# Performance work log

Measured on AMD Instinct MI355X. Metric: run time of the kernel, lower is better.

## Reference

```python
import jax, jax.numpy as jnp
import numpy as np

NUM_ENTITIES = 100000
NUM_RELATIONS = 8
HIDDEN = 128
N_NODES = 100000
N_EDGES = 500000


def setup_inputs() -> dict:
    key = jax.random.key(0)
    ks = jax.random.split(key, 10)
    scale = 1.0 / np.sqrt(HIDDEN)
    inp = {
        "x_ids": jax.random.randint(ks[0], (N_NODES,), 0, NUM_ENTITIES),
        "edge_index": jax.random.randint(ks[1], (2, N_EDGES), 0, N_NODES),
        "edge_type": jax.random.randint(ks[2], (N_EDGES,), 0, NUM_RELATIONS),
        "emb": jax.random.normal(ks[3], (NUM_ENTITIES, HIDDEN), jnp.float32),
        "W1": jax.random.normal(ks[4], (NUM_RELATIONS, HIDDEN, HIDDEN), jnp.float32) * scale,
        "root1": jax.random.normal(ks[5], (HIDDEN, HIDDEN), jnp.float32) * scale,
        "b1": jnp.zeros((HIDDEN,), jnp.float32),
        "W2": jax.random.normal(ks[6], (NUM_RELATIONS, HIDDEN, HIDDEN), jnp.float32) * scale,
        "root2": jax.random.normal(ks[7], (HIDDEN, HIDDEN), jnp.float32) * scale,
        "b2": jnp.zeros((HIDDEN,), jnp.float32),
    }
    return inp


def rgcn_conv(x, edge_index, edge_type, W, root, bias):
    # x: [N, d]; W: [R, d, d]; PyG RGCNConv with aggr='mean' (per-relation mean)
    N, d = x.shape
    R = W.shape[0]
    src, dst = edge_index[0], edge_index[1]
    # transform every node under every relation: [N, R, d]
    h = jnp.einsum('nd,rdf->nrf', x, W)
    msg = h[src, edge_type]                       # [E, d] gather per edge
    seg = dst * R + edge_type                     # composite (node, relation) segment id
    sums = jax.ops.segment_sum(msg, seg, num_segments=N * R)
    cnt = jax.ops.segment_sum(jnp.ones((msg.shape[0], 1), x.dtype), seg, num_segments=N * R)
    agg = (sums / jnp.maximum(cnt, 1.0)).reshape(N, R, d).sum(axis=1)
    return agg + x @ root + bias


def reference(x_ids, edge_index, edge_type, emb, W1, root1, b1, W2, root2, b2):
    x = emb[x_ids]                                # embedding lookup [N, d]
    x = rgcn_conv(x, edge_index, edge_type, W1, root1, b1)
    x = jax.nn.relu(x)
    x = rgcn_conv(x, edge_index, edge_type, W2, root2, b2)
    return jax.nn.sigmoid(x)
```

## Files before the change

kernel.cpp:

```cpp
#include <hip/hip_runtime.h>
#include <hip/hip_bf16.h>

#define HD 128
#define RNUM 8
#define SCAN_BS 2048

typedef __attribute__((ext_vector_type(8))) short short8;
typedef __attribute__((ext_vector_type(4))) float float4e;

__device__ __forceinline__ unsigned short f2bf(float f) {
    unsigned int u = __float_as_uint(f);
    u += 0x7fffu + ((u >> 16) & 1u);
    return (unsigned short)(u >> 16);
}

__device__ __forceinline__ void gload_lds16(const void* g, void* l) {
    __builtin_amdgcn_global_load_lds(
        (const __attribute__((address_space(1))) void*)g,
        (__attribute__((address_space(3))) void*)l, 16, 0, 0);
}

__global__ void zero_i(int* __restrict__ p, int n) {
    int g = blockIdx.x * blockDim.x + threadIdx.x;
    if (g < n) p[g] = 0;
}

__global__ void count_kernel(const int* __restrict__ ei, const int* __restrict__ et,
                             int* __restrict__ cnt, int E, int N) {
    int e = blockIdx.x * blockDim.x + threadIdx.x;
    if (e < E) atomicAdd(&cnt[et[e] * N + ei[E + e]], 1);
}

__global__ void scan1(const int* __restrict__ in, int* __restrict__ out,
                      int* __restrict__ bsum, int n) {
    __shared__ int s[256];
    const int tid = threadIdx.x;
    const int base = blockIdx.x * SCAN_BS + tid * 8;
    int v[8];
    int sum = 0;
#pragma unroll
    for (int j = 0; j < 8; j++) {
        int x = (base + j < n) ? in[base + j] : 0;
        v[j] = sum;
        sum += x;
    }
    s[tid] = sum;
    __syncthreads();
    for (int off = 1; off < 256; off <<= 1) {
        int tv = (tid >= off) ? s[tid - off] : 0;
        __syncthreads();
        if (tid >= off) s[tid] += tv;
        __syncthreads();
    }
    int excl = (tid > 0) ? s[tid - 1] : 0;
    if (tid == 255) bsum[blockIdx.x] = s[255];
#pragma unroll
    for (int j = 0; j < 8; j++)
        if (base + j < n) out[base + j] = v[j] + excl;
}

__global__ void scan2(int* __restrict__ bsum, int nb) {
    __shared__ int s[512];
    const int tid = threadIdx.x;
    s[tid] = (tid < nb) ? bsum[tid] : 0;
    __syncthreads();
    for (int off = 1; off < 512; off <<= 1) {
        int tv = (tid >= off) ? s[tid - off] : 0;
        __syncthreads();
        if (tid >= off) s[tid] += tv;
        __syncthreads();
    }
    if (tid < nb) bsum[tid] = (tid > 0) ? s[tid - 1] : 0;
}

__global__ void scan3(int* __restrict__ out, int* __restrict__ cur,
                      const int* __restrict__ bsum, int n) {
    const int base = blockIdx.x * SCAN_BS + threadIdx.x * 8;
    const int add = bsum[blockIdx.x];
#pragma unroll
    for (int j = 0; j < 8; j++) {
        int i = base + j;
        if (i < n) {
            int v = out[i] + add;
            out[i] = v;
            cur[i] = v;
        }
    }
}

__global__ void fill_kernel(const int* __restrict__ ei, const int* __restrict__ et,
                            const int* __restrict__ ids,
                            int* __restrict__ cur, int* __restrict__ col,
                            int* __restrict__ colE, int E, int N) {
    int e = blockIdx.x * blockDim.x + threadIdx.x;
    if (e < E) {
        int src = ei[e];
        int pos = atomicAdd(&cur[et[e] * N + ei[E + e]], 1);
        col[pos] = src;
        colE[pos] = ids[src];
    }
}

__global__ void wt_kernel(const float* __restrict__ W, unsigned short* __restrict__ WT,
                          int nmat) {
    int g = blockIdx.x * blockDim.x + threadIdx.x;
    if (g >= nmat * 16384) return;
    int mat = g >> 14;
    int d = (g >> 7) & 127;
    int f = g & 127;
    WT[mat * 16384 + f * 128 + d] = f2bf(W[g]);
}

template <bool HAS_IDX, int ACT>
__launch_bounds__(512, 4)
__global__ void rgcn_fused(const int* __restrict__ row_start, const int* __restrict__ col,
                           const int* __restrict__ ids, const float* __restrict__ x,
                           const unsigned short* __restrict__ WT,
                           const float* __restrict__ bias,
                           float* __restrict__ Cout, int N, int E) {
    __shared__ unsigned short As[128 * 128];
    __shared__ unsigned short Ws[128 * 128];

    const int tid = threadIdx.x;
    const int block0 = blockIdx.x * 128;
    const int w = tid >> 6;
    const int lane = tid & 63;
    const int ln15 = lane & 15;
    const int quad = lane >> 4;
    const int rowbase = (w & 1) * 64;
    const int colbase = (w >> 1) * 32;
    const int grp = tid >> 3;
    const int sub8 = tid & 7;

    float4e acc[4][2];
#pragma unroll
    for (int i = 0; i < 4; i++)
#pragma unroll
        for (int j = 0; j < 2; j++)
#pragma unroll
            for (int q = 0; q < 4; q++) acc[i][j][q] = 0.0f;

    for (int s = 0; s < 9; s++) {
        {
            const unsigned short* Wsrc = WT + s * 16384;
#pragma unroll
            for (int i = 0; i < 4; i++) {
                int c = i * 512 + tid;
                int f = c >> 4;
                int cc = c & 15;
                const void* src = (const void*)(Wsrc + f * 128 + ((cc ^ (f & 15)) << 3));
                int cbase = i * 512 + (tid & ~63);
                gload_lds16(src, (char*)Ws + (size_t)cbase * 16);
            }
        }
        if (s < RNUM) {
#pragma unroll 1
            for (int half = 0; half < 2; half++) {
                const int row = grp + half * 64;
                const int dst = block0 + row;
                float4e a0 = {0.f, 0.f, 0.f, 0.f};
                float4e a1 = {0.f, 0.f, 0.f, 0.f};
                float4e a2 = {0.f, 0.f, 0.f, 0.f};
                float4e a3 = {0.f, 0.f, 0.f, 0.f};
                float inv = 0.f;
                if (dst < N) {
                    int seg = s * N + dst;
                    int s0 = row_start[seg];
                    int s1 = (seg == RNUM * N - 1) ? E : row_start[seg + 1];
                    if (s1 > s0) inv = 1.0f / (float)(s1 - s0);
                    for (int e = s0; e < s1; e++) {
                        int c = col[e];
                        const float4e* xp = (const float4e*)(x + (size_t)c * HD + sub8 * 16);
                        a0 += xp[0];
                        a1 += xp[1];
                        a2 += xp[2];
                        a3 += xp[3];
                    }
                }
                a0 *= inv; a1 *= inv; a2 *= inv; a3 *= inv;
                uint4 o0, o1;
                o0.x = (unsigned int)f2bf(a0[0]) | ((unsigned int)f2bf(a0[1]) << 16);
                o0.y = (unsigned int)f2bf(a0[2]) | ((unsigned int)f2bf(a0[3]) << 16);
                o0.z = (unsigned int)f2bf(a1[0]) | ((unsigned int)f2bf(a1[1]) << 16);
                o0.w = (unsigned int)f2bf(a1[2]) | ((unsigned int)f2bf(a1[3]) << 16);
                o1.x = (unsigned int)f2bf(a2[0]) | ((unsigned int)f2bf(a2[1]) << 16);
                o1.y = (unsigned int)f2bf(a2[2]) | ((unsigned int)f2bf(a2[3]) << 16);
                o1.z = (unsigned int)f2bf(a3[0]) | ((unsigned int)f2bf(a3[1]) << 16);
                o1.w = (unsigned int)f2bf(a3[2]) | ((unsigned int)f2bf(a3[3]) << 16);
                const int ck0 = sub8 * 2;
                *(uint4*)&As[row * 128 + ((ck0 ^ (row & 15)) << 3)] = o0;
                *(uint4*)&As[row * 128 + (((ck0 + 1) ^ (row & 15)) << 3)] = o1;
            }
        } else {
#pragma unroll 1
            for (int half = 0; half < 2; half++) {
                const int row = grp + half * 64;
                const int dst = block0 + row;
                uint4 o0 = {0u, 0u, 0u, 0u}, o1 = {0u, 0u, 0u, 0u};
                if (dst < N) {
                    int srcn = HAS_IDX ? ids[dst] : dst;
                    const float* xp = x + (size_t)srcn * HD + sub8 * 16;
                    float4 v0 = *(const float4*)(xp);
                    float4 v1 = *(const float4*)(xp + 4);
                    float4 v2 = *(const float4*)(xp + 8);
                    float4 v3 = *(const float4*)(xp + 12);
                    o0.x = (unsigned int)f2bf(v0.x) | ((unsigned int)f2bf(v0.y) << 16);
                    o0.y = (unsigned int)f2bf(v0.z) | ((unsigned int)f2bf(v0.w) << 16);
                    o0.z = (unsigned int)f2bf(v1.x) | ((unsigned int)f2bf(v1.y) << 16);
                    o0.w = (unsigned int)f2bf(v1.z) | ((unsigned int)f2bf(v1.w) << 16);
                    o1.x = (unsigned int)f2bf(v2.x) | ((unsigned int)f2bf(v2.y) << 16);
                    o1.y = (unsigned int)f2bf(v2.z) | ((unsigned int)f2bf(v2.w) << 16);
                    o1.z = (unsigned int)f2bf(v3.x) | ((unsigned int)f2bf(v3.y) << 16);
                    o1.w = (unsigned int)f2bf(v3.z) | ((unsigned int)f2bf(v3.w) << 16);
                }
                const int ck0 = sub8 * 2;
                *(uint4*)&As[row * 128 + ((ck0 ^ (row & 15)) << 3)] = o0;
                *(uint4*)&As[row * 128 + (((ck0 + 1) ^ (row & 15)) << 3)] = o1;
            }
        }
        __syncthreads();

#pragma unroll
        for (int k0 = 0; k0 < 4; k0++) {
            short8 af[4], bf[2];
#pragma unroll
            for (int rt = 0; rt < 4; rt++) {
                int m = rowbase + rt * 16 + ln15;
                int ck = k0 * 4 + quad;
                af[rt] = *(const short8*)&As[m * 128 + ((ck ^ (m & 15)) << 3)];
            }
#pragma unroll
            for (int ct = 0; ct < 2; ct++) {
                int n = colbase + ct * 16 + ln15;
                int ck = k0 * 4 + quad;
                bf[ct] = *(const short8*)&Ws[n * 128 + ((ck ^ (n & 15)) << 3)];
            }
#pragma unroll
            for (int rt = 0; rt < 4; rt++)
#pragma unroll
                for (int ct = 0; ct < 2; ct++)
                    acc[rt][ct] = __builtin_amdgcn_mfma_f32_16x16x32_bf16(
                        af[rt], bf[ct], acc[rt][ct], 0, 0, 0);
        }
        __syncthreads();
    }

#pragma unroll
    for (int ct = 0; ct < 2; ct++) {
        int ncol = colbase + ct * 16 + ln15;
        float bv = bias[ncol];
#pragma unroll
        for (int rt = 0; rt < 4; rt++) {
#pragma unroll
            for (int rg = 0; rg < 4; rg++) {
                int rowg = block0 + rowbase + rt * 16 + quad * 4 + rg;
                if (rowg < N) {
                    float v = acc[rt][ct][rg] + bv;
                    v = (ACT == 0) ? fmaxf(v, 0.0f) : (1.0f / (1.0f + expf(-v)));
                    Cout[(size_t)rowg * HD + ncol] = v;
                }
            }
        }
    }
}

extern "C" void kernel_launch(void* const* d_in, const int* in_sizes, int n_in,
                              void* d_out, int out_size, void* d_ws, size_t ws_size,
                              hipStream_t stream) {
    const int*   x_ids = (const int*)d_in[0];
    const int*   ei    = (const int*)d_in[1];
    const int*   et    = (const int*)d_in[2];
    const float* emb   = (const float*)d_in[3];
    const float* W1    = (const float*)d_in[4];
    const float* root1 = (const float*)d_in[5];
    const float* b1    = (const float*)d_in[6];
    const float* W2    = (const float*)d_in[7];
    const float* root2 = (const float*)d_in[8];
    const float* b2    = (const float*)d_in[9];

    const int N = in_sizes[0];
    const int E = in_sizes[1] / 2;
    const int NS = RNUM * N;
    float* out = (float*)d_out;

    char* ws = (char*)d_ws;
    size_t off = 0;
    int* row_start = (int*)(ws + off); off += (size_t)NS * 4;
    int* col       = (int*)(ws + off); off += (size_t)E * 4;
    int* colE      = (int*)(ws + off); off += (size_t)E * 4;
    int* bsum      = (int*)(ws + off); off += 4096;
    unsigned short* WT = (unsigned short*)(ws + off); off += (size_t)18 * 16384 * 2;
    float* z       = (float*)(ws + off); off += (size_t)N * HD * 4;
    int* cur       = (int*)z;

    const int scanBlocks = (NS + SCAN_BS - 1) / SCAN_BS;
    const int layerGrid = (N + 127) / 128;

    zero_i<<<(NS + 255) / 256, 256, 0, stream>>>(cur, NS);
    count_kernel<<<(E + 255) / 256, 256, 0, stream>>>(ei, et, cur, E, N);
    scan1<<<scanBlocks, 256, 0, stream>>>(cur, row_start, bsum, NS);
    scan2<<<1, 512, 0, stream>>>(bsum, scanBlocks);
    scan3<<<scanBlocks, 256, 0, stream>>>(row_start, cur, bsum, NS);
    fill_kernel<<<(E + 255) / 256, 256, 0, stream>>>(ei, et, x_ids, cur, col, colE, E, N);

    wt_kernel<<<(8 * 16384 + 255) / 256, 256, 0, stream>>>(W1, WT, 8);
    wt_kernel<<<(1 * 16384 + 255) / 256, 256, 0, stream>>>(root1, WT + 8 * 16384, 1);
    wt_kernel<<<(8 * 16384 + 255) / 256, 256, 0, stream>>>(W2, WT + 9 * 16384, 8);
    wt_kernel<<<(1 * 16384 + 255) / 256, 256, 0, stream>>>(root2, WT + 17 * 16384, 1);

    rgcn_fused<true, 0><<<layerGrid, 512, 0, stream>>>(
        row_start, colE, x_ids, emb, WT, b1, z, N, E);
    rgcn_fused<false, 1><<<layerGrid, 512, 0, stream>>>(
        row_start, col, nullptr, z, WT + 9 * 16384, b2, out, N, E);
}
```

Before: 439.1 us.

## Gather bf16 features, shrink tiles to 64 rows, read weights directly from global

Converts the embedding table to bf16 in a pre-pass and writes the layer-1 output as bf16, so the per-edge neighbour gathers move half the bytes. The fused kernel now uses 64-row tiles with 256 threads and drops the LDS weight staging, reading B fragments straight from global/L2. The four weight-transpose launches are merged into one. The bf16 intermediate adds rounding error, and the extra conversion pass over the full embedding table (100k×128) costs bandwidth.

```diff
diff --git a/kernel.cpp b/kernel.cpp
--- a/kernel.cpp
+++ b/kernel.cpp
@@ -1,5 +1,4 @@
 #include <hip/hip_runtime.h>
-#include <hip/hip_bf16.h>
 
 #define HD 128
 #define RNUM 8
@@ -14,15 +13,28 @@
     return (unsigned short)(u >> 16);
 }
 
-__device__ __forceinline__ void gload_lds16(const void* g, void* l) {
-    __builtin_amdgcn_global_load_lds(
-        (const __attribute__((address_space(1))) void*)g,
-        (__attribute__((address_space(3))) void*)l, 16, 0, 0);
+__device__ __forceinline__ void acc2(float4e& a, unsigned int u, int i) {
+    a[i]     += __uint_as_float(u << 16);
+    a[i + 1] += __uint_as_float(u & 0xffff0000u);
 }
 
 __global__ void zero_i(int* __restrict__ p, int n) {
     int g = blockIdx.x * blockDim.x + threadIdx.x;
     if (g < n) p[g] = 0;
+}
+
+__global__ void tobf16_kernel(const float* __restrict__ in, unsigned short* __restrict__ out,
+                              long long n8) {
+    long long g = (long long)blockIdx.x * blockDim.x + threadIdx.x;
+    if (g >= n8) return;
+    const float4* p = (const float4*)(in + g * 8);
+    float4 v0 = p[0], v1 = p[1];
+    uint4 o;
+    o.x = (unsigned int)f2bf(v0.x) | ((unsigned int)f2bf(v0.y) << 16);
+    o.y = (unsigned int)f2bf(v0.z) | ((unsigned int)f2bf(v0.w) << 16);
+    o.z = (unsigned int)f2bf(v1.x) | ((unsigned int)f2bf(v1.y) << 16);
+    o.w = (unsigned int)f2bf(v1.z) | ((unsigned int)f2bf(v1.w) << 16);
+    *(uint4*)(out + g * 8) = o;
 }
 
 __global__ void count_kernel(const int* __restrict__ ei, const int* __restrict__ et,
@@ -101,62 +113,58 @@
     }
 }
 
-__global__ void wt_kernel(const float* __restrict__ W, unsigned short* __restrict__ WT,
-                          int nmat) {
+__global__ void wt_all(const float* __restrict__ W1, const float* __restrict__ r1,
+                       const float* __restrict__ W2, const float* __restrict__ r2,
+                       unsigned short* __restrict__ WT) {
     int g = blockIdx.x * blockDim.x + threadIdx.x;
-    if (g >= nmat * 16384) return;
+    if (g >= 18 * 16384) return;
     int mat = g >> 14;
-    int d = (g >> 7) & 127;
-    int f = g & 127;
-    WT[mat * 16384 + f * 128 + d] = f2bf(W[g]);
+    int idx = g & 16383;
+    int d = idx >> 7;
+    int f = idx & 127;
+    const float* src;
+    int m;
+    if (mat < 8)       { src = W1; m = mat; }
+    else if (mat == 8) { src = r1; m = 0; }
+    else if (mat < 17) { src = W2; m = mat - 9; }
+    else               { src = r2; m = 0; }
+    WT[mat * 16384 + f * 128 + d] = f2bf(src[(size_t)m * 16384 + d * 128 + f]);
 }
 
 template <bool HAS_IDX, int ACT>
-__launch_bounds__(512, 4)
+__launch_bounds__(256, 6)
 __global__ void rgcn_fused(const int* __restrict__ row_start, const int* __restrict__ col,
-                           const int* __restrict__ ids, const float* __restrict__ x,
+                           const int* __restrict__ ids,
+                           const unsigned short* __restrict__ x16,
                            const unsigned short* __restrict__ WT,
                            const float* __restrict__ bias,
-                           float* __restrict__ Cout, int N, int E) {
-    __shared__ unsigned short As[128 * 128];
-    __shared__ unsigned short Ws[128 * 128];
+                           void* __restrict__ CoutV, int N, int E) {
+    __shared__ unsigned short As[64 * 128];
 
     const int tid = threadIdx.x;
-    const int block0 = blockIdx.x * 128;
+    const int block0 = blockIdx.x * 64;
     const int w = tid >> 6;
     const int lane = tid & 63;
     const int ln15 = lane & 15;
     const int quad = lane >> 4;
-    const int rowbase = (w & 1) * 64;
-    const int colbase = (w >> 1) * 32;
+    const int rowbase = (w & 1) * 32;
+    const int colbase = (w >> 1) * 64;
     const int grp = tid >> 3;
     const int sub8 = tid & 7;
 
-    float4e acc[4][2];
-#pragma unroll
-    for (int i = 0; i < 4; i++)
-#pragma unroll
-        for (int j = 0; j < 2; j++)
+    float4e acc[2][4];
+#pragma unroll
+    for (int i = 0; i < 2; i++)
+#pragma unroll
+        for (int j = 0; j < 4; j++)
 #pragma unroll
             for (int q = 0; q < 4; q++) acc[i][j][q] = 0.0f;
 
     for (int s = 0; s < 9; s++) {
-        {
-            const unsigned short* Wsrc = WT + s * 16384;
-#pragma unroll
-            for (int i = 0; i < 4; i++) {
-                int c = i * 512 + tid;
-                int f = c >> 4;
-                int cc = c & 15;
-                const void* src = (const void*)(Wsrc + f * 128 + ((cc ^ (f & 15)) << 3));
-                int cbase = i * 512 + (tid & ~63);
-                gload_lds16(src, (char*)Ws + (size_t)cbase * 16);
-            }
-        }
         if (s < RNUM) {
 #pragma unroll 1
             for (int half = 0; half < 2; half++) {
-                const int row = grp + half * 64;
+                const int row = grp + half * 32;
                 const int dst = block0 + row;
                 float4e a0 = {0.f, 0.f, 0.f, 0.f};
                 float4e a1 = {0.f, 0.f, 0.f, 0.f};
@@ -170,11 +178,13 @@
                     if (s1 > s0) inv = 1.0f / (float)(s1 - s0);
                     for (int e = s0; e < s1; e++) {
                         int c = col[e];
-                        const float4e* xp = (const float4e*)(x + (size_t)c * HD + sub8 * 16);
-                        a0 += xp[0];
-                        a1 += xp[1];
-                        a2 += xp[2];
-                        a3 += xp[3];
+                        const uint4* xp = (const uint4*)(x16 + (size_t)c * HD + sub8 * 16);
+                        uint4 v0 = xp[0];
+                        uint4 v1 = xp[1];
+                        acc2(a0, v0.x, 0); acc2(a0, v0.y, 2);
+                        acc2(a1, v0.z, 0); acc2(a1, v0.w, 2);
+                        acc2(a2, v1.x, 0); acc2(a2, v1.y, 2);
+                        acc2(a3, v1.z, 0); acc2(a3, v1.w, 2);
                     }
                 }
                 a0 *= inv; a1 *= inv; a2 *= inv; a3 *= inv;
@@ -194,24 +204,14 @@
         } else {
 #pragma unroll 1
             for (int half = 0; half < 2; half++) {
-                const int row = grp + half * 64;
+                const int row = grp + half * 32;
                 const int dst = block0 + row;
                 uint4 o0 = {0u, 0u, 0u, 0u}, o1 = {0u, 0u, 0u, 0u};
                 if (dst < N) {
                     int srcn = HAS_IDX ? ids[dst] : dst;
-                    const float* xp = x + (size_t)srcn * HD + sub8 * 16;
-                    float4 v0 = *(const float4*)(xp);
-                    float4 v1 = *(const float4*)(xp + 4);
-                    float4 v2 = *(const float4*)(xp + 8);
-                    float4 v3 = *(const float4*)(xp + 12);
-                    o0.x = (unsigned int)f2bf(v0.x) | ((unsigned int)f2bf(v0.y) << 16);
-                    o0.y = (unsigned int)f2bf(v0.z) | ((unsigned int)f2bf(v0.w) << 16);
-                    o0.z = (unsigned int)f2bf(v1.x) | ((unsigned int)f2bf(v1.y) << 16);
-                    o0.w = (unsigned int)f2bf(v1.z) | ((unsigned int)f2bf(v1.w) << 16);
-                    o1.x = (unsigned int)f2bf(v2.x) | ((unsigned int)f2bf(v2.y) << 16);
-                    o1.y = (unsigned int)f2bf(v2.z) | ((unsigned int)f2bf(v2.w) << 16);
-                    o1.z = (unsigned int)f2bf(v3.x) | ((unsigned int)f2bf(v3.y) << 16);
-                    o1.w = (unsigned int)f2bf(v3.z) | ((unsigned int)f2bf(v3.w) << 16);
+                    const uint4* xp = (const uint4*)(x16 + (size_t)srcn * HD + sub8 * 16);
+                    o0 = xp[0];
+                    o1 = xp[1];
                 }
                 const int ck0 = sub8 * 2;
                 *(uint4*)&As[row * 128 + ((ck0 ^ (row & 15)) << 3)] = o0;
@@ -220,25 +220,25 @@
         }
         __syncthreads();
 
+        const unsigned short* Wb = WT + s * 16384;
 #pragma unroll
         for (int k0 = 0; k0 < 4; k0++) {
-            short8 af[4], bf[2];
-#pragma unroll
-            for (int rt = 0; rt < 4; rt++) {
+            short8 af[2], bf[4];
+            const int ck = k0 * 4 + quad;
+#pragma unroll
+            for (int rt = 0; rt < 2; rt++) {
                 int m = rowbase + rt * 16 + ln15;
-                int ck = k0 * 4 + quad;
                 af[rt] = *(const short8*)&As[m * 128 + ((ck ^ (m & 15)) << 3)];
             }
 #pragma unroll
-            for (int ct = 0; ct < 2; ct++) {
+            for (int ct = 0; ct < 4; ct++) {
                 int n = colbase + ct * 16 + ln15;
-                int ck = k0 * 4 + quad;
-                bf[ct] = *(const short8*)&Ws[n * 128 + ((ck ^ (n & 15)) << 3)];
-            }
-#pragma unroll
-            for (int rt = 0; rt < 4; rt++)
-#pragma unroll
-                for (int ct = 0; ct < 2; ct++)
+                bf[ct] = *(const short8*)(Wb + n * 128 + ck * 8);
+            }
+#pragma unroll
+            for (int rt = 0; rt < 2; rt++)
+#pragma unroll
+                for (int ct = 0; ct < 4; ct++)
                     acc[rt][ct] = __builtin_amdgcn_mfma_f32_16x16x32_bf16(
                         af[rt], bf[ct], acc[rt][ct], 0, 0, 0);
         }
@@ -246,18 +246,23 @@
     }
 
 #pragma unroll
-    for (int ct = 0; ct < 2; ct++) {
+    for (int ct = 0; ct < 4; ct++) {
         int ncol = colbase + ct * 16 + ln15;
         float bv = bias[ncol];
 #pragma unroll
-        for (int rt = 0; rt < 4; rt++) {
+        for (int rt = 0; rt < 2; rt++) {
 #pragma unroll
             for (int rg = 0; rg < 4; rg++) {
                 int rowg = block0 + rowbase + rt * 16 + quad * 4 + rg;
                 if (rowg < N) {
                     float v = acc[rt][ct][rg] + bv;
-                    v = (ACT == 0) ? fmaxf(v, 0.0f) : (1.0f / (1.0f + expf(-v)));
-                    Cout[(size_t)rowg * HD + ncol] = v;
+                    if (ACT == 0) {
+                        v = fmaxf(v, 0.0f);
+                        ((unsigned short*)CoutV)[(size_t)rowg * HD + ncol] = f2bf(v);
+                    } else {
+                        v = 1.0f / (1.0f + expf(-v));
+                        ((float*)CoutV)[(size_t)rowg * HD + ncol] = v;
+                    }
                 }
             }
         }
@@ -281,6 +286,7 @@
     const int N = in_sizes[0];
     const int E = in_sizes[1] / 2;
     const int NS = RNUM * N;
+    const long long embElems = (long long)in_sizes[3];
     float* out = (float*)d_out;
 
     char* ws = (char*)d_ws;
@@ -289,12 +295,13 @@
     int* col       = (int*)(ws + off); off += (size_t)E * 4;
     int* colE      = (int*)(ws + off); off += (size_t)E * 4;
     int* bsum      = (int*)(ws + off); off += 4096;
-    unsigned short* WT = (unsigned short*)(ws + off); off += (size_t)18 * 16384 * 2;
-    float* z       = (float*)(ws + off); off += (size_t)N * HD * 4;
-    int* cur       = (int*)z;
+    unsigned short* WT    = (unsigned short*)(ws + off); off += (size_t)18 * 16384 * 2;
+    unsigned short* emb16 = (unsigned short*)(ws + off); off += (size_t)embElems * 2;
+    unsigned short* z16   = (unsigned short*)(ws + off); off += (size_t)N * HD * 2;
+    int* cur = (int*)z16;
 
     const int scanBlocks = (NS + SCAN_BS - 1) / SCAN_BS;
-    const int layerGrid = (N + 127) / 128;
+    const int layerGrid = (N + 63) / 64;
 
     zero_i<<<(NS + 255) / 256, 256, 0, stream>>>(cur, NS);
     count_kernel<<<(E + 255) / 256, 256, 0, stream>>>(ei, et, cur, E, N);
@@ -303,13 +310,15 @@
     scan3<<<scanBlocks, 256, 0, stream>>>(row_start, cur, bsum, NS);
     fill_kernel<<<(E + 255) / 256, 256, 0, stream>>>(ei, et, x_ids, cur, col, colE, E, N);
 
-    wt_kernel<<<(8 * 16384 + 255) / 256, 256, 0, stream>>>(W1, WT, 8);
-    wt_kernel<<<(1 * 16384 + 255) / 256, 256, 0, stream>>>(root1, WT + 8 * 16384, 1);
-    wt_kernel<<<(8 * 16384 + 255) / 256, 256, 0, stream>>>(W2, WT + 9 * 16384, 8);
-    wt_kernel<<<(1 * 16384 + 255) / 256, 256, 0, stream>>>(root2, WT + 17 * 16384, 1);
-
-    rgcn_fused<true, 0><<<layerGrid, 512, 0, stream>>>(
-        row_start, colE, x_ids, emb, WT, b1, z, N, E);
-    rgcn_fused<false, 1><<<layerGrid, 512, 0, stream>>>(
-        row_start, col, nullptr, z, WT + 9 * 16384, b2, out, N, E);
-}
+    wt_all<<<(18 * 16384 + 255) / 256, 256, 0, stream>>>(W1, root1, W2, root2, WT);
+
+    {
+        long long n8 = embElems / 8;
+        tobf16_kernel<<<(unsigned int)((n8 + 255) / 256), 256, 0, stream>>>(emb, emb16, n8);
+    }
+
+    rgcn_fused<true, 0><<<layerGrid, 256, 0, stream>>>(
+        row_start, colE, x_ids, emb16, WT, b1, (void*)z16, N, E);
+    rgcn_fused<false, 1><<<layerGrid, 256, 0, stream>>>(
+        row_start, col, nullptr, z16, WT + 9 * 16384, b2, (void*)out, N, E);
+}
```

Result: slower. 573.6 us (+30.6%).
